# Optimization experiments

Hardware: AMD Instinct MI355X
Metric: run time of the kernel (lower is better)

## Reference

```python
import jax, jax.numpy as jnp
import numpy as np

PI = 3.14159265358979323846
MARGIN = 6.0
DIM = 256
ENT_TOT = 43234
REL_RANGE = (6.0 + 2.0) / DIM  # (margin + epsilon) / dim = 0.03125


def setup_inputs() -> dict:
    key = jax.random.key(0)
    k1, k2, k3 = jax.random.split(key, 3)
    head = jax.random.normal(k1, (32, 2 * DIM), dtype=jnp.float32)
    relation = jax.random.normal(k2, (32, DIM), dtype=jnp.float32)
    ent_emb = jax.random.normal(k3, (ENT_TOT, 2 * DIM), dtype=jnp.float32)
    return {"head": head, "relation": relation, "ent_emb": ent_emb}


def reference(head, relation, ent_emb):
    # head: (B, 2D) -> re/im halves (B, D)
    re_h, im_h = jnp.split(head, 2, axis=-1)
    # entity table: (E, 2D) -> (E, D) each
    re_t, im_t = jnp.split(ent_emb, 2, axis=-1)
    # phase rotation from relation embedding
    phase = relation / (REL_RANGE / PI)          # (B, D)
    re_r = jnp.cos(phase)
    im_r = jnp.sin(phase)
    # complex rotation of head by relation: (B, D)
    re_rot = re_h * re_r - im_h * im_r
    im_rot = re_h * im_r + im_h * re_r
    # difference against every entity, broadcast to (B, E, D)
    re_s = re_rot[:, None, :] - re_t[None, :, :]
    im_s = im_rot[:, None, :] - im_t[None, :, :]
    # L2 norm over the complex pair, summed over D -> (B, E)
    dist = jnp.sqrt(re_s * re_s + im_s * im_s).sum(axis=-1)
    return MARGIN - dist
```

## Files before the change

### kernel.cpp

```cpp
#include <hip/hip_runtime.h>
#include <math.h>

#define DIMH 256
#define NB   32
#define E_TOT 43234
#define TE   128
#define DK   32
#define DHALF 128
#define PHASE_DIV 0.009947183943243459f

typedef float v2f __attribute__((ext_vector_type(2)));

__global__ __launch_bounds__(256) void init_kernel(float* __restrict__ out) {
    int i = blockIdx.x * 256 + threadIdx.x;
    if (i < (NB * E_TOT) / 4) {
        float4 v = make_float4(6.0f, 6.0f, 6.0f, 6.0f);
        reinterpret_cast<float4*>(out)[i] = v;
    }
}

__global__ void rot_kernel(const float* __restrict__ head,
                           const float* __restrict__ rel,
                           float* __restrict__ rot) {
    int i = blockIdx.x * blockDim.x + threadIdx.x;
    int b = i >> 8;
    int d = i & 255;
    float re_h = head[b * 2 * DIMH + d];
    float im_h = head[b * 2 * DIMH + DIMH + d];
    float ph = rel[b * DIMH + d] / PHASE_DIV;
    float s, c;
    sincosf(ph, &s, &c);
    rot[b * DIMH + d]             = re_h * c - im_h * s;
    rot[NB * DIMH + b * DIMH + d] = re_h * s + im_h * c;
}

__device__ __forceinline__ v2f sqrt2(v2f s) {
    v2f r;
    r.x = __builtin_amdgcn_sqrtf(s.x);
    r.y = __builtin_amdgcn_sqrtf(s.y);
    return r;
}

__global__ __launch_bounds__(256, 4) void dist_kernel(const float* __restrict__ ent,
                                                      const float* __restrict__ rot,
                                                      float* __restrict__ out) {
    __shared__ float s_er[TE][DK + 2];
    __shared__ float s_ei[TE][DK + 2];
    __shared__ float s_rr[NB][DK + 2];
    __shared__ float s_ri[NB][DK + 2];

    const int tid   = threadIdx.x;
    const int etile = blockIdx.x >> 1;
    const int half  = blockIdx.x & 1;
    const int eb    = etile * TE;
    const int eg    = tid & 31;
    const int bg    = (tid >> 5) * 4;
    const int dbase = half * DHALF;

    v2f acc[4][4];
    #pragma unroll
    for (int j = 0; j < 4; ++j)
        #pragma unroll
        for (int k = 0; k < 4; ++k) { acc[j][k].x = 0.f; acc[j][k].y = 0.f; }

    for (int c = 0; c < DHALF / DK; ++c) {
        const int dk = dbase + c * DK;
        #pragma unroll
        for (int it = 0; it < 4; ++it) {
            int q   = tid + it * 256;
            int row = q >> 3;
            int col = (q & 7) << 2;
            int er  = eb + row;
            if (er >= E_TOT) er = E_TOT - 1;
            const float* base = &ent[(size_t)er * (2 * DIMH)];
            float4 vre = *reinterpret_cast<const float4*>(base + dk + col);
            float4 vim = *reinterpret_cast<const float4*>(base + DIMH + dk + col);
            *reinterpret_cast<float2*>(&s_er[row][col])     = make_float2(vre.x, vre.y);
            *reinterpret_cast<float2*>(&s_er[row][col + 2]) = make_float2(vre.z, vre.w);
            *reinterpret_cast<float2*>(&s_ei[row][col])     = make_float2(vim.x, vim.y);
            *reinterpret_cast<float2*>(&s_ei[row][col + 2]) = make_float2(vim.z, vim.w);
        }
        {
            int row = tid >> 3;
            int col = (tid & 7) << 2;
            float4 vrr = *reinterpret_cast<const float4*>(&rot[row * DIMH + dk + col]);
            float4 vri = *reinterpret_cast<const float4*>(&rot[NB * DIMH + row * DIMH + dk + col]);
            *reinterpret_cast<float2*>(&s_rr[row][col])     = make_float2(vrr.x, vrr.y);
            *reinterpret_cast<float2*>(&s_rr[row][col + 2]) = make_float2(vrr.z, vrr.w);
            *reinterpret_cast<float2*>(&s_ri[row][col])     = make_float2(vri.x, vri.y);
            *reinterpret_cast<float2*>(&s_ri[row][col + 2]) = make_float2(vri.z, vri.w);
        }
        __syncthreads();

        #pragma unroll 2
        for (int d = 0; d < DK; d += 2) {
            v2f rr[4], ri[4], er[4], ei[4];
            #pragma unroll
            for (int j = 0; j < 4; ++j) {
                rr[j] = *reinterpret_cast<const v2f*>(&s_rr[bg + j][d]);
                ri[j] = *reinterpret_cast<const v2f*>(&s_ri[bg + j][d]);
            }
            #pragma unroll
            for (int k = 0; k < 4; ++k) {
                er[k] = *reinterpret_cast<const v2f*>(&s_er[eg + 32 * k][d]);
                ei[k] = *reinterpret_cast<const v2f*>(&s_ei[eg + 32 * k][d]);
            }
            #pragma unroll
            for (int j = 0; j < 4; ++j)
                #pragma unroll
                for (int k = 0; k < 4; ++k) {
                    v2f a = rr[j] - er[k];
                    v2f b = ri[j] - ei[k];
                    v2f s = a * a + b * b;
                    acc[j][k] += sqrt2(s);
                }
        }
        __syncthreads();
    }

    #pragma unroll
    for (int k = 0; k < 4; ++k) {
        int e = eb + eg + 32 * k;
        if (e < E_TOT) {
            #pragma unroll
            for (int j = 0; j < 4; ++j)
                atomicAdd(&out[(size_t)(bg + j) * E_TOT + e],
                          -(acc[j][k].x + acc[j][k].y));
        }
    }
}

extern "C" void kernel_launch(void* const* d_in, const int* in_sizes, int n_in,
                              void* d_out, int out_size, void* d_ws, size_t ws_size,
                              hipStream_t stream) {
    const float* head = (const float*)d_in[0];
    const float* rel  = (const float*)d_in[1];
    const float* ent  = (const float*)d_in[2];
    float* rot = (float*)d_ws;

    int init_blocks = ((NB * E_TOT) / 4 + 255) / 256;
    init_kernel<<<init_blocks, 256, 0, stream>>>((float*)d_out);
    rot_kernel<<<(NB * DIMH) / 256, 256, 0, stream>>>(head, rel, rot);

    int etiles = (E_TOT + TE - 1) / TE;
    dist_kernel<<<etiles * 2, 256, 0, stream>>>(ent, rot, (float*)d_out);
}
```

Baseline: 176.5 us.

## Interleave re/im in shared memory as float4 and split D into quarters

Shared-memory tiles now hold re and im pairs together as float4, so each inner step does one 128-bit LDS read per operand instead of two 64-bit reads. The D dimension is split across four blocks instead of two, doubling the grid to improve parallelism and load balance. Occupancy is lowered to 3 blocks per CU in launch bounds. The trade-off is twice as many atomicAdd operations to the output, plus a different LDS padding that may change bank conflicts.

```diff
diff --git a/kernel.cpp b/kernel.cpp
--- a/kernel.cpp
+++ b/kernel.cpp
@@ -6,10 +6,11 @@
 #define E_TOT 43234
 #define TE   128
 #define DK   32
-#define DHALF 128
+#define DQ   64
 #define PHASE_DIV 0.009947183943243459f
 
 typedef float v2f __attribute__((ext_vector_type(2)));
+typedef float v4f __attribute__((ext_vector_type(4)));
 
 __global__ __launch_bounds__(256) void init_kernel(float* __restrict__ out) {
     int i = blockIdx.x * 256 + threadIdx.x;
@@ -41,21 +42,19 @@
     return r;
 }
 
-__global__ __launch_bounds__(256, 4) void dist_kernel(const float* __restrict__ ent,
+__global__ __launch_bounds__(256, 3) void dist_kernel(const float* __restrict__ ent,
                                                       const float* __restrict__ rot,
                                                       float* __restrict__ out) {
-    __shared__ float s_er[TE][DK + 2];
-    __shared__ float s_ei[TE][DK + 2];
-    __shared__ float s_rr[NB][DK + 2];
-    __shared__ float s_ri[NB][DK + 2];
+    __shared__ v4f s_e[TE][DK / 2 + 1];
+    __shared__ v4f s_r[NB][DK / 2 + 1];
 
     const int tid   = threadIdx.x;
-    const int etile = blockIdx.x >> 1;
-    const int half  = blockIdx.x & 1;
+    const int etile = blockIdx.x >> 2;
+    const int quart = blockIdx.x & 3;
     const int eb    = etile * TE;
     const int eg    = tid & 31;
     const int bg    = (tid >> 5) * 4;
-    const int dbase = half * DHALF;
+    const int dbase = quart * DQ;
 
     v2f acc[4][4];
     #pragma unroll
@@ -63,54 +62,50 @@
         #pragma unroll
         for (int k = 0; k < 4; ++k) { acc[j][k].x = 0.f; acc[j][k].y = 0.f; }
 
-    for (int c = 0; c < DHALF / DK; ++c) {
+    for (int c = 0; c < DQ / DK; ++c) {
         const int dk = dbase + c * DK;
         #pragma unroll
         for (int it = 0; it < 4; ++it) {
             int q   = tid + it * 256;
             int row = q >> 3;
-            int col = (q & 7) << 2;
+            int c4  = q & 7;
             int er  = eb + row;
             if (er >= E_TOT) er = E_TOT - 1;
             const float* base = &ent[(size_t)er * (2 * DIMH)];
-            float4 vre = *reinterpret_cast<const float4*>(base + dk + col);
-            float4 vim = *reinterpret_cast<const float4*>(base + DIMH + dk + col);
-            *reinterpret_cast<float2*>(&s_er[row][col])     = make_float2(vre.x, vre.y);
-            *reinterpret_cast<float2*>(&s_er[row][col + 2]) = make_float2(vre.z, vre.w);
-            *reinterpret_cast<float2*>(&s_ei[row][col])     = make_float2(vim.x, vim.y);
-            *reinterpret_cast<float2*>(&s_ei[row][col + 2]) = make_float2(vim.z, vim.w);
+            float4 vre = *reinterpret_cast<const float4*>(base + dk + 4 * c4);
+            float4 vim = *reinterpret_cast<const float4*>(base + DIMH + dk + 4 * c4);
+            v4f lo, hi;
+            lo.x = vre.x; lo.y = vre.y; lo.z = vim.x; lo.w = vim.y;
+            hi.x = vre.z; hi.y = vre.w; hi.z = vim.z; hi.w = vim.w;
+            s_e[row][2 * c4]     = lo;
+            s_e[row][2 * c4 + 1] = hi;
         }
         {
             int row = tid >> 3;
-            int col = (tid & 7) << 2;
-            float4 vrr = *reinterpret_cast<const float4*>(&rot[row * DIMH + dk + col]);
-            float4 vri = *reinterpret_cast<const float4*>(&rot[NB * DIMH + row * DIMH + dk + col]);
-            *reinterpret_cast<float2*>(&s_rr[row][col])     = make_float2(vrr.x, vrr.y);
-            *reinterpret_cast<float2*>(&s_rr[row][col + 2]) = make_float2(vrr.z, vrr.w);
-            *reinterpret_cast<float2*>(&s_ri[row][col])     = make_float2(vri.x, vri.y);
-            *reinterpret_cast<float2*>(&s_ri[row][col + 2]) = make_float2(vri.z, vri.w);
+            int c4  = tid & 7;
+            float4 vrr = *reinterpret_cast<const float4*>(&rot[row * DIMH + dk + 4 * c4]);
+            float4 vri = *reinterpret_cast<const float4*>(&rot[NB * DIMH + row * DIMH + dk + 4 * c4]);
+            v4f lo, hi;
+            lo.x = vrr.x; lo.y = vrr.y; lo.z = vri.x; lo.w = vri.y;
+            hi.x = vrr.z; hi.y = vrr.w; hi.z = vri.z; hi.w = vri.w;
+            s_r[row][2 * c4]     = lo;
+            s_r[row][2 * c4 + 1] = hi;
         }
         __syncthreads();
 
-        #pragma unroll 2
-        for (int d = 0; d < DK; d += 2) {
-            v2f rr[4], ri[4], er[4], ei[4];
+        #pragma unroll 4
+        for (int p = 0; p < DK / 2; ++p) {
+            v4f r4[4], e4[4];
             #pragma unroll
-            for (int j = 0; j < 4; ++j) {
-                rr[j] = *reinterpret_cast<const v2f*>(&s_rr[bg + j][d]);
-                ri[j] = *reinterpret_cast<const v2f*>(&s_ri[bg + j][d]);
-            }
+            for (int j = 0; j < 4; ++j) r4[j] = s_r[bg + j][p];
             #pragma unroll
-            for (int k = 0; k < 4; ++k) {
-                er[k] = *reinterpret_cast<const v2f*>(&s_er[eg + 32 * k][d]);
-                ei[k] = *reinterpret_cast<const v2f*>(&s_ei[eg + 32 * k][d]);
-            }
+            for (int k = 0; k < 4; ++k) e4[k] = s_e[eg + 32 * k][p];
             #pragma unroll
             for (int j = 0; j < 4; ++j)
                 #pragma unroll
                 for (int k = 0; k < 4; ++k) {
-                    v2f a = rr[j] - er[k];
-                    v2f b = ri[j] - ei[k];
+                    v2f a = r4[j].xy - e4[k].xy;
+                    v2f b = r4[j].zw - e4[k].zw;
                     v2f s = a * a + b * b;
                     acc[j][k] += sqrt2(s);
                 }
@@ -143,5 +138,5 @@
     rot_kernel<<<(NB * DIMH) / 256, 256, 0, stream>>>(head, rel, rot);
 
     int etiles = (E_TOT + TE - 1) / TE;
-    dist_kernel<<<etiles * 2, 256, 0, stream>>>(ent, rot, (float*)d_out);
+    dist_kernel<<<etiles * 4, 256, 0, stream>>>(ent, rot, (float*)d_out);
 }
```

Measured after the change: 178.6 us. Within noise of the previous version (+1.2%).
